# Kernel optimization log

Hardware: AMD Instinct MI355X
Metric: run time of the kernel (lower is better)

## Reference

```python
import jax, jax.numpy as jnp
import numpy as np

B, S, H, Z = 32, 2048, 256, 64
TEMPERATURE = float(H) ** 0.5
NEG_INF = -1e9


def setup_inputs() -> dict:
    key = jax.random.key(0)
    ks = jax.random.split(key, 8)
    return {
        "encoder_hidden_states": jax.random.normal(ks[0], (B, S, H), dtype=jnp.float32),
        "decoder_hidden_states": jax.random.normal(ks[1], (B, S, H), dtype=jnp.float32),
        "decoder_final_hidden_state": jax.random.normal(ks[2], (B, H), dtype=jnp.float32),
        "latent_z_seq": jax.random.normal(ks[3], (B, S, Z), dtype=jnp.float32),
        "mask": jax.random.randint(ks[4], (B, S), 0, 2).astype(bool),
        "Wq": jax.random.normal(ks[5], (H, H), dtype=jnp.float32),
        "Wk": jax.random.normal(ks[6], (H, H), dtype=jnp.float32),
        "Wv": jax.random.normal(ks[7], (Z, Z), dtype=jnp.float32),
    }


def reference(encoder_hidden_states, decoder_hidden_states, decoder_final_hidden_state,
              latent_z_seq, mask, Wq, Wk, Wv):
    # Projections
    k = jnp.einsum('bsh,hd->bsd', encoder_hidden_states, Wk)
    q = jnp.einsum('bsh,hd->bsd', decoder_hidden_states, Wq)
    v = jnp.einsum('bsz,zd->bsd', latent_z_seq, Wv)
    # alignment[b, i, j] = q_i . k_j / sqrt(H)   -> [B, S, S]
    alignment = jnp.einsum('bid,bjd->bij', q, k) / TEMPERATURE
    # mask over QUERY positions (axis -2), broadcast along key axis (-1)
    alignment = jnp.where(mask[:, :, None], alignment, NEG_INF)
    # NOTE: non-standard softmax over the query axis (dim=-2)
    attn = jax.nn.softmax(alignment, axis=-2)
    output = jnp.einsum('bij,bjd->bid', attn, v)  # [B, S, Z]
    return output, attn
```

## Files before the change

### kernel.cpp

```cpp
#include <hip/hip_runtime.h>
#include <stdint.h>

#define B_  32
#define S_  2048
#define H_  256
#define Z_  64

typedef unsigned short u16;
typedef __attribute__((ext_vector_type(8))) short bf16x8;
typedef __attribute__((ext_vector_type(4))) float f32x4;

__device__ __forceinline__ u16 f2bf(float f) {
    unsigned int x = __float_as_uint(f);
    x = (x + 0x7fffu + ((x >> 16) & 1u)) >> 16;
    return (u16)x;
}
__device__ __forceinline__ float bf2f(u16 u) {
    return __uint_as_float(((unsigned int)u) << 16);
}

__device__ __forceinline__ void gl2lds16(const void* g, void* l) {
    __builtin_amdgcn_global_load_lds(
        (const __attribute__((address_space(1))) unsigned int*)g,
        (__attribute__((address_space(3))) unsigned int*)l,
        16, 0, 0);
}

__global__ void detect_kernel(const u16* __restrict__ wq, int* __restrict__ flag) {
    __shared__ int tot;
    const int t = threadIdx.x;
    if (t == 0) tot = 0;
    __syncthreads();
    int cnt = 0;
    #pragma unroll
    for (int r = 0; r < 16; ++r) {
        u16 u = wq[(r * 256 + t) * 2];
        int e = (u >> 7) & 0xFF;
        cnt += (u == 0 || (e >= 107 && e <= 132)) ? 1 : 0;
    }
    atomicAdd(&tot, cnt);
    __syncthreads();
    if (t == 0) *flag = (tot < 2048) ? 1 : 0;
}

__global__ __launch_bounds__(256) void mask_conv_kernel(const void* __restrict__ raw,
                                                        int* __restrict__ mi) {
    __shared__ int isByte;
    const int t = threadIdx.x;
    if (t == 0) isByte = 0;
    __syncthreads();
    const unsigned int* w = (const unsigned int*)raw;
    if (w[t & 255] > 1u) isByte = 1;
    __syncthreads();
    int e = blockIdx.x * 256 + t;
    int val;
    if (isByte) val = ((const unsigned char*)raw)[e] ? 1 : 0;
    else        val = w[e] ? 1 : 0;
    mi[e] = val;
}

__global__ void wsplit_kernel(const int* __restrict__ flagp,
                              const void* __restrict__ Wq, const void* __restrict__ Wk,
                              u16* __restrict__ WqTh, u16* __restrict__ WqTl,
                              u16* __restrict__ WkTh, u16* __restrict__ WkTl) {
    const int fp32 = *flagp;
    const void* src = blockIdx.y ? Wk : Wq;
    u16* oh = blockIdx.y ? WkTh : WqTh;
    u16* ol = blockIdx.y ? WkTl : WqTl;
    int base = blockIdx.x * 1024;
    #pragma unroll
    for (int r = 0; r < 4; ++r) {
        int idx = base + r * 256 + threadIdx.x;
        int d = idx >> 8, h = idx & 255;
        float v = fp32 ? ((const float*)src)[h * 256 + d]
                       : bf2f(((const u16*)src)[h * 256 + d]);
        u16 hi = f2bf(v);
        oh[idx] = hi;
        ol[idx] = f2bf(v - bf2f(hi));
    }
}

__global__ __launch_bounds__(256) void xsplit_kernel(
        const int* __restrict__ flagp,
        const void* __restrict__ dec, const void* __restrict__ enc,
        u16* __restrict__ Xdh, u16* __restrict__ Xdl,
        u16* __restrict__ Xeh, u16* __restrict__ Xel)
{
    const int fp32 = *flagp;
    const void* src = blockIdx.y ? enc : dec;
    u16* oh = blockIdx.y ? Xeh : Xdh;
    u16* ol = blockIdx.y ? Xel : Xdl;
    const int t = threadIdx.x;
    const size_t blockbase = (size_t)blockIdx.x * 4096;
    if (fp32) {
        const float4* s4 = (const float4*)src;
        #pragma unroll
        for (int j = 0; j < 4; ++j) {
            size_t idx = blockbase + j * 1024 + t * 4;
            float4 v = s4[idx >> 2];
            u16 h0 = f2bf(v.x), h1 = f2bf(v.y), h2 = f2bf(v.z), h3 = f2bf(v.w);
            u16 l0 = f2bf(v.x - bf2f(h0)), l1 = f2bf(v.y - bf2f(h1));
            u16 l2 = f2bf(v.z - bf2f(h2)), l3 = f2bf(v.w - bf2f(h3));
            uint2 ph, pl;
            ph.x = (unsigned)h0 | ((unsigned)h1 << 16);
            ph.y = (unsigned)h2 | ((unsigned)h3 << 16);
            pl.x = (unsigned)l0 | ((unsigned)l1 << 16);
            pl.y = (unsigned)l2 | ((unsigned)l3 << 16);
            ((uint2*)oh)[idx >> 2] = ph;
            ((uint2*)ol)[idx >> 2] = pl;
        }
    } else {
        const uint2* s2 = (const uint2*)src;
        #pragma unroll
        for (int j = 0; j < 4; ++j) {
            size_t idx = blockbase + j * 1024 + t * 4;
            uint2 r = s2[idx >> 2];
            uint2 z; z.x = 0u; z.y = 0u;
            ((uint2*)oh)[idx >> 2] = r;
            ((uint2*)ol)[idx >> 2] = z;
        }
    }
}

__global__ __launch_bounds__(256, 2) void proj_kernel(
        const int* __restrict__ flagp, int use_xsplit,
        const float* __restrict__ Xf0, const u16* __restrict__ Xu0,
        const u16* __restrict__ Xh0, const u16* __restrict__ Xl0,
        const u16* __restrict__ WTh0, const u16* __restrict__ WTl0,
        u16* __restrict__ Ph0, u16* __restrict__ Pl0,
        const float* __restrict__ Xf1, const u16* __restrict__ Xu1,
        const u16* __restrict__ Xh1, const u16* __restrict__ Xl1,
        const u16* __restrict__ WTh1, const u16* __restrict__ WTl1,
        u16* __restrict__ Ph1, u16* __restrict__ Pl1)
{
    __shared__ __align__(16) u16 lds[16384];
    const int z = blockIdx.z;
    const float* Xf = z ? Xf1 : Xf0;
    const u16*   Xu = z ? Xu1 : Xu0;
    const u16*   Xh = z ? Xh1 : Xh0;
    const u16*   Xl = z ? Xl1 : Xl0;
    const u16*  WTh = z ? WTh1 : WTh0;
    const u16*  WTl = z ? WTl1 : WTl0;
    u16* Ph = z ? Ph1 : Ph0;
    u16* Pl = z ? Pl1 : Pl0;

    const int fp32 = *flagp;
    const int t = threadIdx.x;
    const int lane = t & 63, w = t >> 6;
    const int i0 = blockIdx.x * 128;
    const int d0 = blockIdx.y * 128;
    const int rh = w >> 1, ch = w & 1;
    const int l15 = lane & 15;
    const int c0 = lane >> 4;

    const int srow = t >> 3;
    const int scp  = t & 7;
    const int sc   = scp ^ (srow & 7);
    const int scol = (sc & 3) * 8;
    const int slo  = sc & 4;

    f32x4 acc[4][4];
    #pragma unroll
    for (int a = 0; a < 4; ++a)
        #pragma unroll
        for (int c = 0; c < 4; ++c) acc[a][c] = (f32x4){0.f, 0.f, 0.f, 0.f};

    for (int ks = 0; ks < 8; ++ks) {
        const int kc = ks * 32;
        {
            const u16* wsrc = slo ? WTl : WTh;
            #pragma unroll
            for (int rep = 0; rep < 4; ++rep) {
                int s = t + rep * 256;
                int row = srow + rep * 32;
                gl2lds16(wsrc + (size_t)(d0 + row) * H_ + kc + scol, lds + 8192 + s * 8);
            }
        }
        if (use_xsplit) {
            const u16* xsrc = slo ? Xl : Xh;
            #pragma unroll
            for (int rep = 0; rep < 4; ++rep) {
                int s = t + rep * 256;
                int row = srow + rep * 32;
                gl2lds16(xsrc + (size_t)(i0 + row) * H_ + kc + scol, lds + s * 8);
            }
        } else if (fp32) {
            #pragma unroll
            for (int rep = 0; rep < 2; ++rep) {
                int s = t + rep * 256;
                int r = s >> 2, c8 = s & 3;
                const float4* src = (const float4*)(Xf + (size_t)(i0 + r) * H_ + kc + c8 * 8);
                float4 x0 = src[0], x1 = src[1];
                float xs[8] = {x0.x, x0.y, x0.z, x0.w, x1.x, x1.y, x1.z, x1.w};
                unsigned hh[8], ll[8];
                #pragma unroll
                for (int j = 0; j < 8; ++j) {
                    u16 hb = f2bf(xs[j]);
                    hh[j] = hb;
                    ll[j] = f2bf(xs[j] - bf2f(hb));
                }
                uint4 ph, pl;
                ph.x = hh[0] | (hh[1] << 16); ph.y = hh[2] | (hh[3] << 16);
                ph.z = hh[4] | (hh[5] << 16); ph.w = hh[6] | (hh[7] << 16);
                pl.x = ll[0] | (ll[1] << 16); pl.y = ll[2] | (ll[3] << 16);
                pl.z = ll[4] | (ll[5] << 16); pl.w = ll[6] | (ll[7] << 16);
                int posH = c8 ^ (r & 7);
                *(uint4*)(lds + r * 64 + posH * 8) = ph;
                *(uint4*)(lds + r * 64 + (posH ^ 4) * 8) = pl;
            }
        } else {
            #pragma unroll
            for (int rep = 0; rep < 2; ++rep) {
                int s = t + rep * 256;
                int r = s >> 2, c8 = s & 3;
                uint4 raw = *(const uint4*)(Xu + (size_t)(i0 + r) * H_ + kc + c8 * 8);
                int posH = c8 ^ (r & 7);
                *(uint4*)(lds + r * 64 + posH * 8) = raw;
                *(uint4*)(lds + r * 64 + (posH ^ 4) * 8) = (uint4){0u, 0u, 0u, 0u};
            }
        }
        __syncthreads();
        bf16x8 ah[4], al[4], bh[4], bl[4];
        #pragma unroll
        for (int f = 0; f < 4; ++f) {
            int ra = rh * 64 + f * 16 + l15;
            int rb = ch * 64 + f * 16 + l15;
            int pa = c0 ^ (ra & 7);
            int pb = c0 ^ (rb & 7);
            ah[f] = *(const bf16x8*)(lds + ra * 64 + pa * 8);
            al[f] = *(const bf16x8*)(lds + ra * 64 + (pa ^ 4) * 8);
            bh[f] = *(const bf16x8*)(lds + 8192 + rb * 64 + pb * 8);
            bl[f] = *(const bf16x8*)(lds + 8192 + rb * 64 + (pb ^ 4) * 8);
        }
        #pragma unroll
        for (int fr = 0; fr < 4; ++fr)
            #pragma unroll
            for (int fc = 0; fc < 4; ++fc) {
                acc[fr][fc] = __builtin_amdgcn_mfma_f32_16x16x32_bf16(al[fr], bh[fc], acc[fr][fc], 0, 0, 0);
                acc[fr][fc] = __builtin_amdgcn_mfma_f32_16x16x32_bf16(ah[fr], bl[fc], acc[fr][fc], 0, 0, 0);
                acc[fr][fc] = __builtin_amdgcn_mfma_f32_16x16x32_bf16(ah[fr], bh[fc], acc[fr][fc], 0, 0, 0);
            }
        __syncthreads();
    }
    #pragma unroll
    for (int fr = 0; fr < 4; ++fr)
        #pragma unroll
        for (int fc = 0; fc < 4; ++fc)
            #pragma unroll
            for (int reg = 0; reg < 4; ++reg) {
                float v = acc[fr][fc][reg];
                int i = i0 + rh * 64 + fr * 16 + (lane >> 4) * 4 + reg;
                int d = d0 + ch * 64 + fc * 16 + l15;
                u16 hi = f2bf(v);
                u16 lo = f2bf(v - bf2f(hi));
                size_t off = (size_t)i * H_ + d;
                Ph[off] = hi;
                Pl[off] = lo;
            }
}

__global__ __launch_bounds__(256) void vproj_kernel(
        const int* __restrict__ flagp, const void* __restrict__ Lraw,
        const void* __restrict__ Wvraw, u16* __restrict__ vT)
{
    __shared__ float wv[64 * 16];
    const int fp32 = *flagp;
    const int t = threadIdx.x;
    const int dc = blockIdx.y;
    #pragma unroll
    for (int r = 0; r < 4; ++r) {
        int idx = r * 256 + t;
        int z = idx >> 4, dd = idx & 15;
        wv[idx] = fp32 ? ((const float*)Wvraw)[z * 64 + dc * 16 + dd]
                       : bf2f(((const u16*)Wvraw)[z * 64 + dc * 16 + dd]);
    }
    __syncthreads();
    const int flat = blockIdx.x * 256 + t;
    const int b = flat >> 11, s = flat & 2047;

    float lz[64];
    if (fp32) {
        const float4* lr = (const float4*)((const float*)Lraw + (size_t)flat * 64);
        #pragma unroll
        for (int c = 0; c < 16; ++c) {
            float4 v = lr[c];
            lz[c * 4 + 0] = v.x; lz[c * 4 + 1] = v.y;
            lz[c * 4 + 2] = v.z; lz[c * 4 + 3] = v.w;
        }
    } else {
        const uint4* lr = (const uint4*)((const u16*)Lraw + (size_t)flat * 64);
        #pragma unroll
        for (int c = 0; c < 8; ++c) {
            uint4 v = lr[c];
            unsigned wd[4] = {v.x, v.y, v.z, v.w};
            #pragma unroll
            for (int e2 = 0; e2 < 4; ++e2) {
                lz[c * 8 + e2 * 2 + 0] = bf2f((u16)(wd[e2] & 0xffffu));
                lz[c * 8 + e2 * 2 + 1] = bf2f((u16)(wd[e2] >> 16));
            }
        }
    }

    float acc[16];
    #pragma unroll
    for (int d = 0; d < 16; ++d) acc[d] = 0.f;
    for (int z = 0; z < 64; ++z) {
        float lv = lz[z];
        const float4* wrow = (const float4*)&wv[z * 16];
        #pragma unroll
        for (int d4 = 0; d4 < 4; ++d4) {
            float4 wq = wrow[d4];
            acc[d4 * 4 + 0] += lv * wq.x;
            acc[d4 * 4 + 1] += lv * wq.y;
            acc[d4 * 4 + 2] += lv * wq.z;
            acc[d4 * 4 + 3] += lv * wq.w;
        }
    }
    #pragma unroll
    for (int d = 0; d < 16; ++d)
        vT[((size_t)b * 64 + dc * 16 + d) * S_ + s] = f2bf(acc[d]);
}

__global__ __launch_bounds__(256, 2) void qk_kernel(
        const u16* __restrict__ qh, const u16* __restrict__ ql,
        const u16* __restrict__ kh, const u16* __restrict__ kl,
        const int* __restrict__ maskI, u16* __restrict__ attnB,
        float* __restrict__ attnF, u16* __restrict__ stageB, int use_stage,
        float* __restrict__ m_p, float* __restrict__ s_p,
        int b0, const int* __restrict__ flagp)
{
    __shared__ __align__(16) char smem[35328];
    u16*  stage = (u16*)smem;
    u16*  etile = (u16*)smem;
    float* cmax = (float*)(smem + 32768);
    float* csum = (float*)(smem + 33792);
    float* mrow = (float*)(smem + 34816);

    const int fp32 = *flagp;
    const int t = threadIdx.x;
    const int lane = t & 63, w = t >> 6;
    const int jt = blockIdx.x, it = blockIdx.y, bz = blockIdx.z;
    const int b = b0 + bz;
    const int i0 = it * 128, j0 = jt * 128;
    const int rh = w >> 1, ch = w & 1;
    const int l15 = lane & 15;
    const int c0 = lane >> 4;

    if (t < 128) mrow[t] = (maskI[b * S_ + i0 + t] != 0) ? 1.f : 0.f;

    const size_t qbase = ((size_t)bz * S_ + i0) * H_;
    const size_t kbase = ((size_t)bz * S_ + j0) * H_;

    const int srow = t >> 3;
    const int scp  = t & 7;
    const int sc   = scp ^ (srow & 7);
    const int scol = (sc & 3) * 8;
    const u16* qsrc = (sc & 4) ? ql : qh;
    const u16* ksrc = (sc & 4) ? kl : kh;

    f32x4 acc[4][4];
    #pragma unroll
    for (int a = 0; a < 4; ++a)
        #pragma unroll
        for (int c = 0; c < 4; ++c) acc[a][c] = (f32x4){0.f, 0.f, 0.f, 0.f};

    for (int ks = 0; ks < 8; ++ks) {
        const int kc = ks * 32;
        #pragma unroll
        for (int rep = 0; rep < 4; ++rep) {
            int s = t + rep * 256;
            int row = srow + rep * 32;
            gl2lds16(qsrc + qbase + (size_t)row * H_ + kc + scol, stage + s * 8);
            gl2lds16(ksrc + kbase + (size_t)row * H_ + kc + scol, stage + 8192 + s * 8);
        }
        __syncthreads();
        bf16x8 ah[4], al[4], bh[4], bl[4];
        #pragma unroll
        for (int f = 0; f < 4; ++f) {
            int ra = rh * 64 + f * 16 + l15;
            int rb = ch * 64 + f * 16 + l15;
            int pa = c0 ^ (ra & 7);
            int pb = c0 ^ (rb & 7);
            ah[f] = *(const bf16x8*)(stage + ra * 64 + pa * 8);
            al[f] = *(const bf16x8*)(stage + ra * 64 + (pa ^ 4) * 8);
            bh[f] = *(const bf16x8*)(stage + 8192 + rb * 64 + pb * 8);
            bl[f] = *(const bf16x8*)(stage + 8192 + rb * 64 + (pb ^ 4) * 8);
        }
        #pragma unroll
        for (int fr = 0; fr < 4; ++fr)
            #pragma unroll
            for (int fc = 0; fc < 4; ++fc) {
                acc[fr][fc] = __builtin_amdgcn_mfma_f32_16x16x32_bf16(al[fr], bh[fc], acc[fr][fc], 0, 0, 0);
                acc[fr][fc] = __builtin_amdgcn_mfma_f32_16x16x32_bf16(ah[fr], bl[fc], acc[fr][fc], 0, 0, 0);
                acc[fr][fc] = __builtin_amdgcn_mfma_f32_16x16x32_bf16(ah[fr], bh[fc], acc[fr][fc], 0, 0, 0);
            }
        __syncthreads();
    }

    const float inv_t = 0.0625f;
    float mloc[4] = {-3e38f, -3e38f, -3e38f, -3e38f};
    #pragma unroll
    for (int fr = 0; fr < 4; ++fr)
        #pragma unroll
        for (int reg = 0; reg < 4; ++reg) {
            float keep = mrow[rh * 64 + fr * 16 + (lane >> 4) * 4 + reg];
            #pragma unroll
            for (int fc = 0; fc < 4; ++fc) {
                float l = acc[fr][fc][reg] * inv_t;
                l = (keep != 0.f) ? l : -1e9f;
                acc[fr][fc][reg] = l;
                mloc[fc] = fmaxf(mloc[fc], l);
            }
        }
    #pragma unroll
    for (int fc = 0; fc < 4; ++fc) {
        mloc[fc] = fmaxf(mloc[fc], __shfl_xor(mloc[fc], 16, 64));
        mloc[fc] = fmaxf(mloc[fc], __shfl_xor(mloc[fc], 32, 64));
    }
    if (lane < 16) {
        #pragma unroll
        for (int fc = 0; fc < 4; ++fc)
            cmax[rh * 128 + ch * 64 + fc * 16 + lane] = mloc[fc];
    }
    __syncthreads();

    float mcol[4], sloc[4];
    #pragma unroll
    for (int fc = 0; fc < 4; ++fc) {
        int c = ch * 64 + fc * 16 + l15;
        mcol[fc] = fmaxf(cmax[c], cmax[128 + c]);
        sloc[fc] = 0.f;
    }
    #pragma unroll
    for (int fr = 0; fr < 4; ++fr)
        #pragma unroll
        for (int reg = 0; reg < 4; ++reg) {
            int row = rh * 64 + fr * 16 + (lane >> 4) * 4 + reg;
            #pragma unroll
            for (int fc = 0; fc < 4; ++fc) {
                float e = __expf(acc[fr][fc][reg] - mcol[fc]);
                sloc[fc] += e;
                etile[row * 128 + ch * 64 + fc * 16 + l15] = f2bf(e);
            }
        }
    #pragma unroll
    for (int fc = 0; fc < 4; ++fc) {
        sloc[fc] += __shfl_xor(sloc[fc], 16, 64);
        sloc[fc] += __shfl_xor(sloc[fc], 32, 64);
    }
    if (lane < 16) {
        #pragma unroll
        for (int fc = 0; fc < 4; ++fc)
            csum[rh * 128 + ch * 64 + fc * 16 + lane] = sloc[fc];
    }
    __syncthreads();

    if (t < 128) {
        float m = fmaxf(cmax[t], cmax[128 + t]);
        float sres = csum[t] + csum[128 + t];
        size_t so = ((size_t)b * 16 + it) * S_ + j0 + t;
        m_p[so] = m;
        s_p[so] = sres;
    }
    const size_t abase = ((size_t)b * S_ + i0) * S_ + j0;
    if (fp32) {
        if (use_stage) {
            #pragma unroll
            for (int rep = 0; rep < 8; ++rep) {
                int s = t + rep * 256;
                int row = s >> 4, off = (s & 15) * 8;
                *(uint4*)(stageB + abase + (size_t)row * S_ + off) = *(const uint4*)(etile + s * 8);
            }
        } else {
            #pragma unroll
            for (int rep = 0; rep < 8; ++rep) {
                int s = t + rep * 256;
                int row = s >> 4, off = (s & 15) * 8;
                const u16* src = etile + s * 8;
                float* gp = attnF + abase + (size_t)row * S_ + off;
                float4 f0, f1;
                f0.x = bf2f(src[0]); f0.y = bf2f(src[1]); f0.z = bf2f(src[2]); f0.w = bf2f(src[3]);
                f1.x = bf2f(src[4]); f1.y = bf2f(src[5]); f1.z = bf2f(src[6]); f1.w = bf2f(src[7]);
                *(float4*)gp = f0;
                *(float4*)(gp + 4) = f1;
            }
        }
    } else {
        #pragma unroll
        for (int rep = 0; rep < 8; ++rep) {
            int s = t + rep * 256;
            int row = s >> 4, off = (s & 15) * 8;
            *(uint4*)(attnB + abase + (size_t)row * S_ + off) = *(const uint4*)(etile + s * 8);
        }
    }
}

__global__ __launch_bounds__(256) void stats_kernel(
        const float* __restrict__ m_p, const float* __restrict__ s_p, float* __restrict__ scl)
{
    int id = blockIdx.x * 256 + threadIdx.x;
    int b = id >> 11, j = id & 2047;
    float mv[16];
    float M = -3e38f;
    #pragma unroll
    for (int itile = 0; itile < 16; ++itile) {
        mv[itile] = m_p[((size_t)b * 16 + itile) * S_ + j];
        M = fmaxf(M, mv[itile]);
    }
    float L = 0.f;
    #pragma unroll
    for (int itile = 0; itile < 16; ++itile)
        L += s_p[((size_t)b * 16 + itile) * S_ + j] * __expf(mv[itile] - M);
    float invL = (L > 0.f) ? (1.f / L) : 0.f;
    #pragma unroll
    for (int itile = 0; itile < 16; ++itile)
        scl[((size_t)b * 16 + itile) * S_ + j] = __expf(mv[itile] - M) * invL;
}

__global__ __launch_bounds__(256, 2) void av_gemm_kernel(
        const u16* __restrict__ vT, const float* __restrict__ scl,
        const u16* __restrict__ stageB, const u16* __restrict__ attnRawB,
        u16* __restrict__ outB, float* __restrict__ outF,
        const int* __restrict__ flagp)
{
    __shared__ __align__(16) u16 lds_attn[128 * 128];
    __shared__ __align__(16) u16 lds_vt[64 * 128];
    const int fp32 = *flagp;
    const u16* srcE = fp32 ? stageB : attnRawB;
    const int t = threadIdx.x;
    const int lane = t & 63, w = t >> 6;
    const int it = blockIdx.x, b = blockIdx.y;
    const int i0 = it * 128;
    const int l15 = lane & 15;

    const int acp = t & 15;
    const int arow0 = t >> 4;
    const int ac = acp ^ (arow0 & 15);
    const int vpos = (t & 15) ^ (t >> 4);
    const int j8 = (t & 15) * 8;

    f32x4 acc[2][4];
    #pragma unroll
    for (int a = 0; a < 2; ++a)
        #pragma unroll
        for (int c = 0; c < 4; ++c) acc[a][c] = (f32x4){0.f, 0.f, 0.f, 0.f};

    for (int jt = 0; jt < 16; ++jt) {
        const int j0 = jt * 128;
        __syncthreads();
        const size_t abase = ((size_t)b * S_ + i0) * S_ + j0;
        #pragma unroll
        for (int rep = 0; rep < 8; ++rep) {
            int s = t + rep * 256;
            int row = arow0 + rep * 16;
            gl2lds16(srcE + abase + (size_t)row * S_ + ac * 8, lds_attn + s * 8);
        }
        float sc[8];
        {
            const float4* sp = (const float4*)(scl + ((size_t)b * 16 + it) * S_ + j0 + j8);
            float4 s0 = sp[0], s1 = sp[1];
            sc[0] = s0.x; sc[1] = s0.y; sc[2] = s0.z; sc[3] = s0.w;
            sc[4] = s1.x; sc[5] = s1.y; sc[6] = s1.z; sc[7] = s1.w;
        }
        #pragma unroll
        for (int rep = 0; rep < 4; ++rep) {
            int d = (t >> 4) + rep * 16;
            uint4 raw = *(const uint4*)(vT + ((size_t)b * 64 + d) * S_ + j0 + j8);
            unsigned wd[4] = {raw.x, raw.y, raw.z, raw.w};
            #pragma unroll
            for (int e2 = 0; e2 < 4; ++e2) {
                float f0 = bf2f((u16)(wd[e2] & 0xffffu)) * sc[e2 * 2];
                float f1 = bf2f((u16)(wd[e2] >> 16))     * sc[e2 * 2 + 1];
                wd[e2] = (unsigned)f2bf(f0) | ((unsigned)f2bf(f1) << 16);
            }
            uint4 pk; pk.x = wd[0]; pk.y = wd[1]; pk.z = wd[2]; pk.w = wd[3];
            *(uint4*)(lds_vt + d * 128 + vpos * 8) = pk;
        }
        __syncthreads();

        #pragma unroll
        for (int ksj = 0; ksj < 4; ++ksj) {
            int ck = ksj * 4 + (lane >> 4);
            int pA = ck ^ l15;
            int rA0 = w * 32 + l15, rA1 = w * 32 + 16 + l15;
            bf16x8 a0 = *(const bf16x8*)(lds_attn + rA0 * 128 + pA * 8);
            bf16x8 a1 = *(const bf16x8*)(lds_attn + rA1 * 128 + pA * 8);
            bf16x8 bb[4];
            #pragma unroll
            for (int fc = 0; fc < 4; ++fc) {
                int d = fc * 16 + l15;
                bb[fc] = *(const bf16x8*)(lds_vt + d * 128 + pA * 8);
            }
            #pragma unroll
            for (int fc = 0; fc < 4; ++fc) {
                acc[0][fc] = __builtin_amdgcn_mfma_f32_16x16x32_bf16(a0, bb[fc], acc[0][fc], 0, 0, 0);
                acc[1][fc] = __builtin_amdgcn_mfma_f32_16x16x32_bf16(a1, bb[fc], acc[1][fc], 0, 0, 0);
            }
        }
    }
    #pragma unroll
    for (int fr = 0; fr < 2; ++fr)
        #pragma unroll
        for (int fc = 0; fc < 4; ++fc)
            #pragma unroll
            for (int reg = 0; reg < 4; ++reg) {
                int i = i0 + w * 32 + fr * 16 + (lane >> 4) * 4 + reg;
                int d = fc * 16 + l15;
                float v = acc[fr][fc][reg];
                size_t oo = ((size_t)b * S_ + i) * Z_ + d;
                if (fp32) outF[oo] = v;
                else      outB[oo] = f2bf(v);
            }
}

__global__ __launch_bounds__(256) void scale_attn_kernel(
        const u16* stageB, u16* attnB, float* attnF,
        const float* __restrict__ scl, const int* __restrict__ flagp)
{
    const int fp32 = *flagp;
    const u16* srcE = fp32 ? stageB : attnB;
    const size_t N8 = (size_t)B_ * S_ * S_ / 8;
    const size_t stride = (size_t)gridDim.x * 256;
    for (size_t u = (size_t)blockIdx.x * 256 + threadIdx.x; u < N8; u += stride) {
        size_t flat = u * 8;
        int j  = (int)(flat & (S_ - 1));
        int i  = (int)((flat >> 11) & (S_ - 1));
        int b  = (int)(flat >> 22);
        int it = i >> 7;
        const float* sp = scl + ((size_t)b * 16 + it) * S_ + j;
        float4 s0 = *(const float4*)sp;
        float4 s1 = *(const float4*)(sp + 4);
        uint4 e = *(const uint4*)(srcE + flat);
        unsigned wd[4] = {e.x, e.y, e.z, e.w};
        float f[8];
        f[0] = bf2f((u16)(wd[0] & 0xffffu)) * s0.x;
        f[1] = bf2f((u16)(wd[0] >> 16))     * s0.y;
        f[2] = bf2f((u16)(wd[1] & 0xffffu)) * s0.z;
        f[3] = bf2f((u16)(wd[1] >> 16))     * s0.w;
        f[4] = bf2f((u16)(wd[2] & 0xffffu)) * s1.x;
        f[5] = bf2f((u16)(wd[2] >> 16))     * s1.y;
        f[6] = bf2f((u16)(wd[3] & 0xffffu)) * s1.z;
        f[7] = bf2f((u16)(wd[3] >> 16))     * s1.w;
        if (fp32) {
            float4 o0, o1;
            o0.x = f[0]; o0.y = f[1]; o0.z = f[2]; o0.w = f[3];
            o1.x = f[4]; o1.y = f[5]; o1.z = f[6]; o1.w = f[7];
            *(float4*)(attnF + flat) = o0;
            *(float4*)(attnF + flat + 4) = o1;
        } else {
            uint4 o;
            o.x = (unsigned)f2bf(f[0]) | ((unsigned)f2bf(f[1]) << 16);
            o.y = (unsigned)f2bf(f[2]) | ((unsigned)f2bf(f[3]) << 16);
            o.z = (unsigned)f2bf(f[4]) | ((unsigned)f2bf(f[5]) << 16);
            o.w = (unsigned)f2bf(f[6]) | ((unsigned)f2bf(f[7]) << 16);
            *(uint4*)(attnB + flat) = o;
        }
    }
}

__global__ __launch_bounds__(256, 2) void av_fallback_kernel(
        const u16* __restrict__ vT, const float* __restrict__ scl,
        u16* __restrict__ attnB, float* __restrict__ attnF,
        u16* __restrict__ outB, float* __restrict__ outF,
        const int* __restrict__ flagp)
{
    __shared__ __align__(16) u16 lds_attn[128 * 128];
    __shared__ __align__(16) u16 lds_vt[64 * 128];
    __shared__ float lds_scale[128];
    const int fp32 = *flagp;
    const int t = threadIdx.x;
    const int lane = t & 63, w = t >> 6;
    const int it = blockIdx.x, b = blockIdx.y;
    const int i0 = it * 128;
    const int l15 = lane & 15, koff = (lane >> 4) * 8;

    f32x4 acc[2][4];
    #pragma unroll
    for (int a = 0; a < 2; ++a)
        #pragma unroll
        for (int c = 0; c < 4; ++c) acc[a][c] = (f32x4){0.f, 0.f, 0.f, 0.f};

    for (int jt = 0; jt < 16; ++jt) {
        const int j0 = jt * 128;
        __syncthreads();
        if (t < 128) lds_scale[t] = scl[((size_t)b * 16 + it) * S_ + j0 + t];
        #pragma unroll
        for (int rep = 0; rep < 4; ++rep) {
            int s = t + rep * 256;
            int d = s >> 4, off = (s & 15) * 8;
            gl2lds16(vT + ((size_t)b * 64 + d) * S_ + j0 + off, lds_vt + s * 8);
        }
        __syncthreads();

        const size_t abase = ((size_t)b * S_ + i0) * S_ + j0;
        if (fp32) {
            #pragma unroll
            for (int rep = 0; rep < 8; ++rep) {
                int s = t + rep * 256;
                int row = s >> 4, off = (s & 15) * 8;
                float* gp = attnF + abase + (size_t)row * S_ + off;
                float4 p0 = *(const float4*)gp;
                float4 p1 = *(const float4*)(gp + 4);
                p0.x *= lds_scale[off + 0]; p0.y *= lds_scale[off + 1];
                p0.z *= lds_scale[off + 2]; p0.w *= lds_scale[off + 3];
                p1.x *= lds_scale[off + 4]; p1.y *= lds_scale[off + 5];
                p1.z *= lds_scale[off + 6]; p1.w *= lds_scale[off + 7];
                *(float4*)gp = p0;
                *(float4*)(gp + 4) = p1;
                uint4 pk;
                pk.x = (unsigned)f2bf(p0.x) | ((unsigned)f2bf(p0.y) << 16);
                pk.y = (unsigned)f2bf(p0.z) | ((unsigned)f2bf(p0.w) << 16);
                pk.z = (unsigned)f2bf(p1.x) | ((unsigned)f2bf(p1.y) << 16);
                pk.w = (unsigned)f2bf(p1.z) | ((unsigned)f2bf(p1.w) << 16);
                *(uint4*)(lds_attn + s * 8) = pk;
            }
        } else {
            #pragma unroll
            for (int rep = 0; rep < 8; ++rep) {
                int s = t + rep * 256;
                int row = s >> 4, off = (s & 15) * 8;
                size_t ga = abase + (size_t)row * S_ + off;
                uint4 pk = *(const uint4*)(attnB + ga);
                unsigned int wd[4] = {pk.x, pk.y, pk.z, pk.w};
                #pragma unroll
                for (int e2 = 0; e2 < 4; ++e2) {
                    float f0 = bf2f((u16)(wd[e2] & 0xffffu)) * lds_scale[off + e2 * 2];
                    float f1 = bf2f((u16)(wd[e2] >> 16))     * lds_scale[off + e2 * 2 + 1];
                    wd[e2] = (unsigned int)f2bf(f0) | ((unsigned int)f2bf(f1) << 16);
                }
                uint4 opk; opk.x = wd[0]; opk.y = wd[1]; opk.z = wd[2]; opk.w = wd[3];
                *(uint4*)(attnB + ga) = opk;
                *(uint4*)(lds_attn + s * 8) = opk;
            }
        }
        __syncthreads();

        #pragma unroll
        for (int ksj = 0; ksj < 4; ++ksj) {
            bf16x8 a0 = *(const bf16x8*)(lds_attn + (w * 32 +  0 + l15) * 128 + ksj * 32 + koff);
            bf16x8 a1 = *(const bf16x8*)(lds_attn + (w * 32 + 16 + l15) * 128 + ksj * 32 + koff);
            bf16x8 bb[4];
            #pragma unroll
            for (int fc = 0; fc < 4; ++fc)
                bb[fc] = *(const bf16x8*)(lds_vt + (fc * 16 + l15) * 128 + ksj * 32 + koff);
            #pragma unroll
            for (int fc = 0; fc < 4; ++fc) {
                acc[0][fc] = __builtin_amdgcn_mfma_f32_16x16x32_bf16(a0, bb[fc], acc[0][fc], 0, 0, 0);
                acc[1][fc] = __builtin_amdgcn_mfma_f32_16x16x32_bf16(a1, bb[fc], acc[1][fc], 0, 0, 0);
            }
        }
    }
    #pragma unroll
    for (int fr = 0; fr < 2; ++fr)
        #pragma unroll
        for (int fc = 0; fc < 4; ++fc)
            #pragma unroll
            for (int reg = 0; reg < 4; ++reg) {
                int i = i0 + w * 32 + fr * 16 + (lane >> 4) * 4 + reg;
                int d = fc * 16 + l15;
                float v = acc[fr][fc][reg];
                size_t oo = ((size_t)b * S_ + i) * Z_ + d;
                if (fp32) outF[oo] = v;
                else      outB[oo] = f2bf(v);
            }
}

extern "C" void kernel_launch(void* const* d_in, const int* in_sizes, int n_in,
                              void* d_out, int out_size, void* d_ws, size_t ws_size,
                              hipStream_t stream) {
    const void* enc    = d_in[0];
    const void* dec    = d_in[1];
    const void* latent = d_in[3];
    const void* mraw   = d_in[4];
    const void* Wq     = d_in[5];
    const void* Wk     = d_in[6];
    const void* Wv     = d_in[7];

    u16*   outB  = (u16*)d_out;
    float* outF  = (float*)d_out;
    u16*   attnB = outB + (size_t)B_ * S_ * Z_;
    float* attnF = outF + (size_t)B_ * S_ * Z_;
    float* m_p = (float*)d_out;
    float* s_p = m_p + (size_t)B_ * 16 * S_;

    char* ws = (char*)d_ws;
    int*   flag  = (int*)ws;
    int*   maskI = (int*)(ws + 256);
    u16*   vT    = (u16*)((char*)maskI + (size_t)B_ * S_ * 4);
    u16*   WqTh  = vT + (size_t)B_ * Z_ * S_;
    u16*   WqTl  = WqTh + H_ * H_;
    u16*   WkTh  = WqTl + H_ * H_;
    u16*   WkTl  = WkTh + H_ * H_;
    float* scl   = (float*)(WkTl + H_ * H_);
    char*  dyn   = (char*)(scl + (size_t)B_ * 16 * S_);

    const size_t fixed_bytes  = (size_t)(dyn - ws);
    const size_t per_batch    = (size_t)4 * S_ * H_ * 2;
    const size_t xsplit_bytes = (size_t)4 * B_ * S_ * H_ * 2;
    const size_t stage_bytes  = (size_t)B_ * S_ * S_ * 2;

    long long avail = (long long)ws_size - (long long)fixed_bytes;
    int use_xsplit = 0, use_stage = 0;
    u16 *Xdh = 0, *Xdl = 0, *Xeh = 0, *Xel = 0, *stageB = 0;
    if (avail >= (long long)(xsplit_bytes + per_batch)) {
        use_xsplit = 1;
        Xdh = (u16*)dyn;
        Xdl = Xdh + (size_t)B_ * S_ * H_;
        Xeh = Xdl + (size_t)B_ * S_ * H_;
        Xel = Xeh + (size_t)B_ * S_ * H_;
        dyn += xsplit_bytes;
        avail -= (long long)xsplit_bytes;
    }
    if (avail >= (long long)(stage_bytes + per_batch)) {
        use_stage = 1;
        stageB = (u16*)dyn;
        dyn += stage_bytes;
        avail -= (long long)stage_bytes;
    }
    int g_b = (avail > 0) ? (int)(avail / (long long)per_batch) : 1;
    if (g_b < 1)  g_b = 1;
    if (g_b > 32) g_b = 32;

    u16* qh = (u16*)dyn;
    u16* ql = qh + (size_t)g_b * S_ * H_;
    u16* kh = ql + (size_t)g_b * S_ * H_;
    u16* kl = kh + (size_t)g_b * S_ * H_;

    detect_kernel<<<dim3(1), 256, 0, stream>>>((const u16*)Wq, flag);
    mask_conv_kernel<<<dim3(256), 256, 0, stream>>>(mraw, maskI);
    wsplit_kernel<<<dim3(64, 2), 256, 0, stream>>>(flag, Wq, Wk, WqTh, WqTl, WkTh, WkTl);
    vproj_kernel<<<dim3(256, 4), 256, 0, stream>>>(flag, latent, Wv, vT);
    if (use_xsplit)
        xsplit_kernel<<<dim3(4096, 2), 256, 0, stream>>>(flag, dec, enc, Xdh, Xdl, Xeh, Xel);

    for (int b0 = 0; b0 < B_; b0 += g_b) {
        int g = (B_ - b0 < g_b) ? (B_ - b0) : g_b;
        size_t eoff = (size_t)b0 * S_ * H_;
        proj_kernel<<<dim3(g * 16, 2, 2), 256, 0, stream>>>(
            flag, use_xsplit,
            (const float*)dec + eoff, (const u16*)dec + eoff,
            use_xsplit ? Xdh + eoff : (u16*)0, use_xsplit ? Xdl + eoff : (u16*)0,
            WqTh, WqTl, qh, ql,
            (const float*)enc + eoff, (const u16*)enc + eoff,
            use_xsplit ? Xeh + eoff : (u16*)0, use_xsplit ? Xel + eoff : (u16*)0,
            WkTh, WkTl, kh, kl);
        qk_kernel<<<dim3(16, 16, g), 256, 0, stream>>>(qh, ql, kh, kl, maskI,
                                                       attnB, attnF, stageB, use_stage,
                                                       m_p, s_p, b0, flag);
    }
    stats_kernel<<<dim3(256), 256, 0, stream>>>(m_p, s_p, scl);
    if (use_stage) {
        av_gemm_kernel<<<dim3(16, 32), 256, 0, stream>>>(vT, scl, stageB, attnB,
                                                         outB, outF, flag);
        scale_attn_kernel<<<dim3(2048), 256, 0, stream>>>(stageB, attnB, attnF, scl, flag);
    } else {
        av_fallback_kernel<<<dim3(16, 32), 256, 0, stream>>>(vT, scl, attnB, attnF,
                                                             outB, outF, flag);
    }
}
```

Before: 1.211 ms.

## Fuse prep kernels into one launch and fold attn scaling into AV GEMM

Four preprocessing kernels (mask conversion, weight split, V projection, input split) are merged into one prep_kernel that picks a role from blockIdx, cutting launch count and letting the small jobs overlap. The separate scale_attn pass is removed. The AV GEMM now rescales the staged attention tile it already holds in LDS and writes the final attn output, so the big B×S×S attention array is not read a second time. The cost is that av_gemm does extra global stores inside its main loop, and the merged kernel may hurt occupancy because each role keeps its own shared-memory arrays.

```diff
diff --git a/kernel.cpp b/kernel.cpp
--- a/kernel.cpp
+++ b/kernel.cpp
@@ -43,8 +43,7 @@
     if (t == 0) *flag = (tot < 2048) ? 1 : 0;
 }
 
-__global__ __launch_bounds__(256) void mask_conv_kernel(const void* __restrict__ raw,
-                                                        int* __restrict__ mi) {
+__device__ void role_mask(int bx, const void* __restrict__ raw, int* __restrict__ mi) {
     __shared__ int isByte;
     const int t = threadIdx.x;
     if (t == 0) isByte = 0;
@@ -52,22 +51,21 @@
     const unsigned int* w = (const unsigned int*)raw;
     if (w[t & 255] > 1u) isByte = 1;
     __syncthreads();
-    int e = blockIdx.x * 256 + t;
+    int e = bx * 256 + t;
     int val;
     if (isByte) val = ((const unsigned char*)raw)[e] ? 1 : 0;
     else        val = w[e] ? 1 : 0;
     mi[e] = val;
 }
 
-__global__ void wsplit_kernel(const int* __restrict__ flagp,
-                              const void* __restrict__ Wq, const void* __restrict__ Wk,
-                              u16* __restrict__ WqTh, u16* __restrict__ WqTl,
-                              u16* __restrict__ WkTh, u16* __restrict__ WkTl) {
-    const int fp32 = *flagp;
-    const void* src = blockIdx.y ? Wk : Wq;
-    u16* oh = blockIdx.y ? WkTh : WqTh;
-    u16* ol = blockIdx.y ? WkTl : WqTl;
-    int base = blockIdx.x * 1024;
+__device__ void role_wsplit(int bx, int by, int fp32,
+                            const void* __restrict__ Wq, const void* __restrict__ Wk,
+                            u16* __restrict__ WqTh, u16* __restrict__ WqTl,
+                            u16* __restrict__ WkTh, u16* __restrict__ WkTl) {
+    const void* src = by ? Wk : Wq;
+    u16* oh = by ? WkTh : WqTh;
+    u16* ol = by ? WkTl : WqTl;
+    int base = bx * 1024;
     #pragma unroll
     for (int r = 0; r < 4; ++r) {
         int idx = base + r * 256 + threadIdx.x;
@@ -80,18 +78,15 @@
     }
 }
 
-__global__ __launch_bounds__(256) void xsplit_kernel(
-        const int* __restrict__ flagp,
-        const void* __restrict__ dec, const void* __restrict__ enc,
-        u16* __restrict__ Xdh, u16* __restrict__ Xdl,
-        u16* __restrict__ Xeh, u16* __restrict__ Xel)
-{
-    const int fp32 = *flagp;
-    const void* src = blockIdx.y ? enc : dec;
-    u16* oh = blockIdx.y ? Xeh : Xdh;
-    u16* ol = blockIdx.y ? Xel : Xdl;
+__device__ void role_xsplit(int bx, int by, int fp32,
+                            const void* __restrict__ dec, const void* __restrict__ enc,
+                            u16* __restrict__ Xdh, u16* __restrict__ Xdl,
+                            u16* __restrict__ Xeh, u16* __restrict__ Xel) {
+    const void* src = by ? enc : dec;
+    u16* oh = by ? Xeh : Xdh;
+    u16* ol = by ? Xel : Xdl;
     const int t = threadIdx.x;
-    const size_t blockbase = (size_t)blockIdx.x * 4096;
+    const size_t blockbase = (size_t)bx * 4096;
     if (fp32) {
         const float4* s4 = (const float4*)src;
         #pragma unroll
@@ -120,6 +115,97 @@
             ((uint2*)ol)[idx >> 2] = z;
         }
     }
+}
+
+__device__ void role_vproj(int bx, int dc, int fp32,
+                           const void* __restrict__ Lraw,
+                           const void* __restrict__ Wvraw, u16* __restrict__ vT) {
+    __shared__ float wv[64 * 16];
+    const int t = threadIdx.x;
+    #pragma unroll
+    for (int r = 0; r < 4; ++r) {
+        int idx = r * 256 + t;
+        int z = idx >> 4, dd = idx & 15;
+        wv[idx] = fp32 ? ((const float*)Wvraw)[z * 64 + dc * 16 + dd]
+                       : bf2f(((const u16*)Wvraw)[z * 64 + dc * 16 + dd]);
+    }
+    __syncthreads();
+    const int flat = bx * 256 + t;
+    const int b = flat >> 11, s = flat & 2047;
+
+    float lz[64];
+    if (fp32) {
+        const float4* lr = (const float4*)((const float*)Lraw + (size_t)flat * 64);
+        #pragma unroll
+        for (int c = 0; c < 16; ++c) {
+            float4 v = lr[c];
+            lz[c * 4 + 0] = v.x; lz[c * 4 + 1] = v.y;
+            lz[c * 4 + 2] = v.z; lz[c * 4 + 3] = v.w;
+        }
+    } else {
+        const uint4* lr = (const uint4*)((const u16*)Lraw + (size_t)flat * 64);
+        #pragma unroll
+        for (int c = 0; c < 8; ++c) {
+            uint4 v = lr[c];
+            unsigned wd[4] = {v.x, v.y, v.z, v.w};
+            #pragma unroll
+            for (int e2 = 0; e2 < 4; ++e2) {
+                lz[c * 8 + e2 * 2 + 0] = bf2f((u16)(wd[e2] & 0xffffu));
+                lz[c * 8 + e2 * 2 + 1] = bf2f((u16)(wd[e2] >> 16));
+            }
+        }
+    }
+
+    float acc[16];
+    #pragma unroll
+    for (int d = 0; d < 16; ++d) acc[d] = 0.f;
+    for (int z = 0; z < 64; ++z) {
+        float lv = lz[z];
+        const float4* wrow = (const float4*)&wv[z * 16];
+        #pragma unroll
+        for (int d4 = 0; d4 < 4; ++d4) {
+            float4 wq = wrow[d4];
+            acc[d4 * 4 + 0] += lv * wq.x;
+            acc[d4 * 4 + 1] += lv * wq.y;
+            acc[d4 * 4 + 2] += lv * wq.z;
+            acc[d4 * 4 + 3] += lv * wq.w;
+        }
+    }
+    #pragma unroll
+    for (int d = 0; d < 16; ++d)
+        vT[((size_t)b * 64 + dc * 16 + d) * S_ + s] = f2bf(acc[d]);
+}
+
+__global__ __launch_bounds__(256) void prep_kernel(
+        const int* __restrict__ flagp, int n_xs,
+        const void* __restrict__ dec, const void* __restrict__ enc,
+        u16* __restrict__ Xdh, u16* __restrict__ Xdl,
+        u16* __restrict__ Xeh, u16* __restrict__ Xel,
+        const void* __restrict__ Lraw, const void* __restrict__ Wvraw,
+        u16* __restrict__ vT,
+        const void* __restrict__ Wq, const void* __restrict__ Wk,
+        u16* __restrict__ WqTh, u16* __restrict__ WqTl,
+        u16* __restrict__ WkTh, u16* __restrict__ WkTl,
+        const void* __restrict__ mraw, int* __restrict__ maskI)
+{
+    const int fp32 = *flagp;
+    int r = blockIdx.x;
+    if (r < n_xs) {
+        role_xsplit(r & 4095, r >> 12, fp32, dec, enc, Xdh, Xdl, Xeh, Xel);
+        return;
+    }
+    r -= n_xs;
+    if (r < 1024) {
+        role_vproj(r & 255, r >> 8, fp32, Lraw, Wvraw, vT);
+        return;
+    }
+    r -= 1024;
+    if (r < 128) {
+        role_wsplit(r & 63, r >> 6, fp32, Wq, Wk, WqTh, WqTl, WkTh, WkTl);
+        return;
+    }
+    r -= 128;
+    role_mask(r, mraw, maskI);
 }
 
 __global__ __launch_bounds__(256, 2) void proj_kernel(
@@ -259,68 +345,6 @@
             }
 }
 
-__global__ __launch_bounds__(256) void vproj_kernel(
-        const int* __restrict__ flagp, const void* __restrict__ Lraw,
-        const void* __restrict__ Wvraw, u16* __restrict__ vT)
-{
-    __shared__ float wv[64 * 16];
-    const int fp32 = *flagp;
-    const int t = threadIdx.x;
-    const int dc = blockIdx.y;
-    #pragma unroll
-    for (int r = 0; r < 4; ++r) {
-        int idx = r * 256 + t;
-        int z = idx >> 4, dd = idx & 15;
-        wv[idx] = fp32 ? ((const float*)Wvraw)[z * 64 + dc * 16 + dd]
-                       : bf2f(((const u16*)Wvraw)[z * 64 + dc * 16 + dd]);
-    }
-    __syncthreads();
-    const int flat = blockIdx.x * 256 + t;
-    const int b = flat >> 11, s = flat & 2047;
-
-    float lz[64];
-    if (fp32) {
-        const float4* lr = (const float4*)((const float*)Lraw + (size_t)flat * 64);
-        #pragma unroll
-        for (int c = 0; c < 16; ++c) {
-            float4 v = lr[c];
-            lz[c * 4 + 0] = v.x; lz[c * 4 + 1] = v.y;
-            lz[c * 4 + 2] = v.z; lz[c * 4 + 3] = v.w;
-        }
-    } else {
-        const uint4* lr = (const uint4*)((const u16*)Lraw + (size_t)flat * 64);
-        #pragma unroll
-        for (int c = 0; c < 8; ++c) {
-            uint4 v = lr[c];
-            unsigned wd[4] = {v.x, v.y, v.z, v.w};
-            #pragma unroll
-            for (int e2 = 0; e2 < 4; ++e2) {
-                lz[c * 8 + e2 * 2 + 0] = bf2f((u16)(wd[e2] & 0xffffu));
-                lz[c * 8 + e2 * 2 + 1] = bf2f((u16)(wd[e2] >> 16));
-            }
-        }
-    }
-
-    float acc[16];
-    #pragma unroll
-    for (int d = 0; d < 16; ++d) acc[d] = 0.f;
-    for (int z = 0; z < 64; ++z) {
-        float lv = lz[z];
-        const float4* wrow = (const float4*)&wv[z * 16];
-        #pragma unroll
-        for (int d4 = 0; d4 < 4; ++d4) {
-            float4 wq = wrow[d4];
-            acc[d4 * 4 + 0] += lv * wq.x;
-            acc[d4 * 4 + 1] += lv * wq.y;
-            acc[d4 * 4 + 2] += lv * wq.z;
-            acc[d4 * 4 + 3] += lv * wq.w;
-        }
-    }
-    #pragma unroll
-    for (int d = 0; d < 16; ++d)
-        vT[((size_t)b * 64 + dc * 16 + d) * S_ + s] = f2bf(acc[d]);
-}
-
 __global__ __launch_bounds__(256, 2) void qk_kernel(
         const u16* __restrict__ qh, const u16* __restrict__ ql,
         const u16* __restrict__ kh, const u16* __restrict__ kl,
@@ -519,14 +543,15 @@
 
 __global__ __launch_bounds__(256, 2) void av_gemm_kernel(
         const u16* __restrict__ vT, const float* __restrict__ scl,
-        const u16* __restrict__ stageB, const u16* __restrict__ attnRawB,
+        const u16* __restrict__ stageB, u16* __restrict__ attnB,
+        float* __restrict__ attnF,
         u16* __restrict__ outB, float* __restrict__ outF,
         const int* __restrict__ flagp)
 {
     __shared__ __align__(16) u16 lds_attn[128 * 128];
     __shared__ __align__(16) u16 lds_vt[64 * 128];
     const int fp32 = *flagp;
-    const u16* srcE = fp32 ? stageB : attnRawB;
+    const u16* srcE = fp32 ? stageB : attnB;
     const int t = threadIdx.x;
     const int lane = t & 63, w = t >> 6;
     const int it = blockIdx.x, b = blockIdx.y;
@@ -555,12 +580,16 @@
             int row = arow0 + rep * 16;
             gl2lds16(srcE + abase + (size_t)row * S_ + ac * 8, lds_attn + s * 8);
         }
-        float sc[8];
+        float sc[8], esc[8];
         {
             const float4* sp = (const float4*)(scl + ((size_t)b * 16 + it) * S_ + j0 + j8);
             float4 s0 = sp[0], s1 = sp[1];
             sc[0] = s0.x; sc[1] = s0.y; sc[2] = s0.z; sc[3] = s0.w;
             sc[4] = s1.x; sc[5] = s1.y; sc[6] = s1.z; sc[7] = s1.w;
+            const float4* ep = (const float4*)(scl + ((size_t)b * 16 + it) * S_ + j0 + ac * 8);
+            float4 e0 = ep[0], e1 = ep[1];
+            esc[0] = e0.x; esc[1] = e0.y; esc[2] = e0.z; esc[3] = e0.w;
+            esc[4] = e1.x; esc[5] = e1.y; esc[6] = e1.z; esc[7] = e1.w;
         }
         #pragma unroll
         for (int rep = 0; rep < 4; ++rep) {
@@ -577,6 +606,38 @@
             *(uint4*)(lds_vt + d * 128 + vpos * 8) = pk;
         }
         __syncthreads();
+
+        #pragma unroll
+        for (int rep = 0; rep < 8; ++rep) {
+            int s = t + rep * 256;
+            int row = arow0 + rep * 16;
+            uint4 pk = *(const uint4*)(lds_attn + s * 8);
+            unsigned wd[4] = {pk.x, pk.y, pk.z, pk.w};
+            float f[8];
+            f[0] = bf2f((u16)(wd[0] & 0xffffu)) * esc[0];
+            f[1] = bf2f((u16)(wd[0] >> 16))     * esc[1];
+            f[2] = bf2f((u16)(wd[1] & 0xffffu)) * esc[2];
+            f[3] = bf2f((u16)(wd[1] >> 16))     * esc[3];
+            f[4] = bf2f((u16)(wd[2] & 0xffffu)) * esc[4];
+            f[5] = bf2f((u16)(wd[2] >> 16))     * esc[5];
+            f[6] = bf2f((u16)(wd[3] & 0xffffu)) * esc[6];
+            f[7] = bf2f((u16)(wd[3] >> 16))     * esc[7];
+            size_t ga = abase + (size_t)row * S_ + ac * 8;
+            if (fp32) {
+                float4 o0, o1;
+                o0.x = f[0]; o0.y = f[1]; o0.z = f[2]; o0.w = f[3];
+                o1.x = f[4]; o1.y = f[5]; o1.z = f[6]; o1.w = f[7];
+                *(float4*)(attnF + ga) = o0;
+                *(float4*)(attnF + ga + 4) = o1;
+            } else {
+                uint4 o;
+                o.x = (unsigned)f2bf(f[0]) | ((unsigned)f2bf(f[1]) << 16);
+                o.y = (unsigned)f2bf(f[2]) | ((unsigned)f2bf(f[3]) << 16);
+                o.z = (unsigned)f2bf(f[4]) | ((unsigned)f2bf(f[5]) << 16);
+                o.w = (unsigned)f2bf(f[6]) | ((unsigned)f2bf(f[7]) << 16);
+                *(uint4*)(attnB + ga) = o;
+            }
+        }
 
         #pragma unroll
         for (int ksj = 0; ksj < 4; ++ksj) {
@@ -611,51 +672,6 @@
                 if (fp32) outF[oo] = v;
                 else      outB[oo] = f2bf(v);
             }
-}
-
-__global__ __launch_bounds__(256) void scale_attn_kernel(
-        const u16* stageB, u16* attnB, float* attnF,
-        const float* __restrict__ scl, const int* __restrict__ flagp)
-{
-    const int fp32 = *flagp;
-    const u16* srcE = fp32 ? stageB : attnB;
-    const size_t N8 = (size_t)B_ * S_ * S_ / 8;
-    const size_t stride = (size_t)gridDim.x * 256;
-    for (size_t u = (size_t)blockIdx.x * 256 + threadIdx.x; u < N8; u += stride) {
-        size_t flat = u * 8;
-        int j  = (int)(flat & (S_ - 1));
-        int i  = (int)((flat >> 11) & (S_ - 1));
-        int b  = (int)(flat >> 22);
-        int it = i >> 7;
-        const float* sp = scl + ((size_t)b * 16 + it) * S_ + j;
-        float4 s0 = *(const float4*)sp;
-        float4 s1 = *(const float4*)(sp + 4);
-        uint4 e = *(const uint4*)(srcE + flat);
-        unsigned wd[4] = {e.x, e.y, e.z, e.w};
-        float f[8];
-        f[0] = bf2f((u16)(wd[0] & 0xffffu)) * s0.x;
-        f[1] = bf2f((u16)(wd[0] >> 16))     * s0.y;
-        f[2] = bf2f((u16)(wd[1] & 0xffffu)) * s0.z;
-        f[3] = bf2f((u16)(wd[1] >> 16))     * s0.w;
-        f[4] = bf2f((u16)(wd[2] & 0xffffu)) * s1.x;
-        f[5] = bf2f((u16)(wd[2] >> 16))     * s1.y;
-        f[6] = bf2f((u16)(wd[3] & 0xffffu)) * s1.z;
-        f[7] = bf2f((u16)(wd[3] >> 16))     * s1.w;
-        if (fp32) {
-            float4 o0, o1;
-            o0.x = f[0]; o0.y = f[1]; o0.z = f[2]; o0.w = f[3];
-            o1.x = f[4]; o1.y = f[5]; o1.z = f[6]; o1.w = f[7];
-            *(float4*)(attnF + flat) = o0;
-            *(float4*)(attnF + flat + 4) = o1;
-        } else {
-            uint4 o;
-            o.x = (unsigned)f2bf(f[0]) | ((unsigned)f2bf(f[1]) << 16);
-            o.y = (unsigned)f2bf(f[2]) | ((unsigned)f2bf(f[3]) << 16);
-            o.z = (unsigned)f2bf(f[4]) | ((unsigned)f2bf(f[5]) << 16);
-            o.w = (unsigned)f2bf(f[6]) | ((unsigned)f2bf(f[7]) << 16);
-            *(uint4*)(attnB + flat) = o;
-        }
-    }
 }
 
 __global__ __launch_bounds__(256, 2) void av_fallback_kernel(
@@ -827,11 +843,11 @@
     u16* kl = kh + (size_t)g_b * S_ * H_;
 
     detect_kernel<<<dim3(1), 256, 0, stream>>>((const u16*)Wq, flag);
-    mask_conv_kernel<<<dim3(256), 256, 0, stream>>>(mraw, maskI);
-    wsplit_kernel<<<dim3(64, 2), 256, 0, stream>>>(flag, Wq, Wk, WqTh, WqTl, WkTh, WkTl);
-    vproj_kernel<<<dim3(256, 4), 256, 0, stream>>>(flag, latent, Wv, vT);
-    if (use_xsplit)
-        xsplit_kernel<<<dim3(4096, 2), 256, 0, stream>>>(flag, dec, enc, Xdh, Xdl, Xeh, Xel);
+
+    const int n_xs = use_xsplit ? 8192 : 0;
+    prep_kernel<<<dim3(n_xs + 1024 + 128 + 256), 256, 0, stream>>>(
+        flag, n_xs, dec, enc, Xdh, Xdl, Xeh, Xel,
+        latent, Wv, vT, Wq, Wk, WqTh, WqTl, WkTh, WkTl, mraw, maskI);
 
     for (int b0 = 0; b0 < B_; b0 += g_b) {
         int g = (B_ - b0 < g_b) ? (B_ - b0) : g_b;
@@ -850,9 +866,8 @@
     }
     stats_kernel<<<dim3(256), 256, 0, stream>>>(m_p, s_p, scl);
     if (use_stage) {
-        av_gemm_kernel<<<dim3(16, 32), 256, 0, stream>>>(vT, scl, stageB, attnB,
+        av_gemm_kernel<<<dim3(16, 32), 256, 0, stream>>>(vT, scl, stageB, attnB, attnF,
                                                          outB, outF, flag);
-        scale_attn_kernel<<<dim3(2048), 256, 0, stream>>>(stageB, attnB, attnF, scl, flag);
     } else {
         av_fallback_kernel<<<dim3(16, 32), 256, 0, stream>>>(vT, scl, attnB, attnF,
                                                              outB, outF, flag);
```

Result: faster. 1.106 ms (-8.7%).
